# Optimization experiments

Hardware: AMD Instinct MI355X
Metric: run time of the kernel (lower is better)

## Reference

```python
import jax, jax.numpy as jnp
import numpy as np
from jax.scipy.linalg import cho_solve, solve_triangular

O = 9            # observations per timestep
L1S1, L1S2 = 3, 1
L = L1S1 + L1S2  # latent dim = 4
N, NT = 4096, 400
JITTER = 1e-6
EPS = 1e-9
LOG2PI = float(np.log(2.0 * np.pi))


def setup_inputs():
    key = jax.random.key(0)
    ks = jax.random.split(key, 9)
    return {
        "y": jax.random.normal(ks[0], (N, NT, O), jnp.float32),
        "B1_state1": 0.3 * jax.random.normal(ks[1], (L1S1, L1S1), jnp.float32),
        "B1_state2": 0.3 * jax.random.normal(ks[2], (L1S2, L1S2), jnp.float32),
        "lambda_r1_free": 0.8 + 0.1 * jax.random.normal(ks[3], (6,), jnp.float32),
        "lambda_r2_free": 0.8 + 0.1 * jax.random.normal(ks[4], (8,), jnp.float32),
        "log_q_diag": 0.1 * jax.random.normal(ks[5], (L,), jnp.float32),
        "log_r_diag": 0.1 * jax.random.normal(ks[6], (O,), jnp.float32),
        "gamma_intercept": 0.5 + 0.1 * jax.random.normal(ks[7], (1,), jnp.float32),
        "gamma_coeffs": 0.1 * jax.random.normal(ks[8], (3,), jnp.float32),
    }


def _build_matrices(B1_state1, B1_state2, l1f, l2f, log_q, log_r):
    B = (jnp.zeros((L, L), jnp.float32)
         .at[:L1S1, :L1S1].set(B1_state1)
         .at[L1S1:, L1S1:].set(B1_state2))
    Q = jnp.diag(jnp.exp(log_q))
    R = jnp.diag(jnp.exp(log_r))
    L1 = (jnp.zeros((O, L), jnp.float32)
          .at[0, 0].set(1.0).at[1, 0].set(l1f[0]).at[2, 0].set(l1f[1])
          .at[3, 1].set(1.0).at[4, 1].set(l1f[2]).at[5, 1].set(l1f[3])
          .at[6, 2].set(1.0).at[7, 2].set(l1f[4]).at[8, 2].set(l1f[5]))
    L2 = jnp.zeros((O, L), jnp.float32).at[0, L1S1].set(1.0).at[1:, L1S1].set(l2f)
    return B, Q, R, L1, L2


def _imm_kf(y, B1_state1, B1_state2, lambda_r1_free, lambda_r2_free,
            log_q_diag, log_r_diag, gamma_intercept, gamma_coeffs):
    n = y.shape[0]
    B, Q, R, L1, L2 = _build_matrices(B1_state1, B1_state2, lambda_r1_free,
                                      lambda_r2_free, log_q_diag, log_r_diag)
    eyeL = jnp.eye(L, dtype=jnp.float32)
    eyeO = jnp.eye(O, dtype=jnp.float32)

    def regime_update(y_t, eta_pred, P_pred, Lm):
        # One regime's Kalman update + Gaussian log-likelihood of the innovation.
        v = y_t - eta_pred @ Lm.T                        # [N,O]
        LP = jnp.einsum('oi,nij->noj', Lm, P_pred)       # [N,O,L]
        F = LP @ Lm.T + R + JITTER * eyeO                # [N,O,O] innovation cov
        c = jnp.linalg.cholesky(F)
        z = solve_triangular(c, v[..., None], lower=True)[..., 0]
        log_lik = (-0.5 * O * LOG2PI
                   - jnp.log(jnp.diagonal(c, axis1=-2, axis2=-1)).sum(-1)
                   - 0.5 * (z * z).sum(-1))              # [N]
        # K = P_pred L^T F^{-1}; F symmetric so K^T = F^{-1} L P_pred
        K = jnp.swapaxes(cho_solve((c, True), LP), -1, -2)   # [N,L,O]
        eta_u = eta_pred + (K @ v[..., None])[..., 0]
        A = eyeL - K @ Lm                                # Joseph form
        P_u = (A @ P_pred @ jnp.swapaxes(A, -1, -2)
               + jnp.einsum('nlo,op,nmp->nlm', K, R, K))
        return log_lik, eta_u, P_u

    def step(carry, y_t):
        prob, eta, P, ll = carry
        p11 = jax.nn.sigmoid(gamma_intercept[0] + eta[:, :L1S1] @ gamma_coeffs)
        eta_pred = eta @ B.T                             # [N,L]
        P_pred = jnp.einsum('ij,njk,lk->nil', B, P, B) + Q
        ll1, eta1, P1 = regime_update(y_t, eta_pred, P_pred, L1)
        ll2, eta2, P2 = regime_update(y_t, eta_pred, P_pred, L2)
        num1 = jnp.exp(ll1) * (prob[:, 0] * p11)                        # p21 = 0
        num2 = jnp.exp(ll2) * (prob[:, 0] * (1.0 - p11) + prob[:, 1])   # p22 = 1
        marg = num1 + num2 + EPS
        pr1, pr2 = num1 / marg, num2 / marg
        ll = ll + jnp.log(marg).sum()
        eta_t = pr1[:, None] * eta1 + pr2[:, None] * eta2
        d1 = (eta1 - eta_t)[..., None]
        d2 = (eta2 - eta_t)[..., None]
        P_t = (pr1[:, None, None] * (P1 + d1 @ jnp.swapaxes(d1, -1, -2))
               + pr2[:, None, None] * (P2 + d2 @ jnp.swapaxes(d2, -1, -2)))
        P_t = 0.5 * (P_t + jnp.swapaxes(P_t, -1, -2))
        probs_t = jnp.stack([pr1, pr2], axis=-1)
        y_pred = pr1[:, None] * (eta_t @ L1.T) + pr2[:, None] * (eta_t @ L2.T)
        return (probs_t, eta_t, P_t, ll), (probs_t, y_pred)

    prob0 = jnp.broadcast_to(jnp.array([0.99, 0.01], jnp.float32), (n, 2))
    eta0 = jnp.zeros((n, L), jnp.float32)
    P0 = jnp.broadcast_to(1000.0 * eyeL, (n, L, L))
    (_, _, _, ll), (probs, y_pred) = jax.lax.scan(
        step, (prob0, eta0, P0, jnp.asarray(0.0, jnp.float32)),
        jnp.swapaxes(y, 0, 1))
    # (neg log-likelihood, filtered_probs [N,Nt,2], predicted_y [N,Nt,O])
    return -ll, jnp.swapaxes(probs, 0, 1), jnp.swapaxes(y_pred, 0, 1)


def reference(y, B1_state1, B1_state2, lambda_r1_free, lambda_r2_free,
              log_q_diag, log_r_diag, gamma_intercept, gamma_coeffs):
    return _imm_kf(y, B1_state1, B1_state2, lambda_r1_free, lambda_r2_free,
                   log_q_diag, log_r_diag, gamma_intercept, gamma_coeffs)
```

## Files before the change

### kernel.cpp

```cpp
#include <hip/hip_runtime.h>
#include <math.h>

#define N_PART 4096
#define N_T    400
#define N_O    9
#define NJ     (N_T*N_O)
#define TT     20
#define LOG2PI_F 1.8378770664093453f

typedef float v2f __attribute__((ext_vector_type(2)));

__device__ __forceinline__ v2f v2exp(v2f x){ v2f r; r.x=__expf(x.x); r.y=__expf(x.y); return r; }
__device__ __forceinline__ v2f v2log(v2f x){ v2f r; r.x=__logf(x.x); r.y=__logf(x.y); return r; }
__device__ __forceinline__ v2f v2rcp(v2f x){ v2f r; r.x=__builtin_amdgcn_rcpf(x.x); r.y=__builtin_amdgcn_rcpf(x.y); return r; }

__global__ __launch_bounds__(256)
void transpose_kernel(const float* __restrict__ y, float* __restrict__ yt,
                      float* __restrict__ ll_ws)
{
    __shared__ float tile[64][65];
    if (blockIdx.x == 0 && blockIdx.y == 0 && threadIdx.x == 0) ll_ws[0] = 0.0f;
    const int j0 = blockIdx.x * 64;
    const int n0 = blockIdx.y * 64;
    const int c  = threadIdx.x & 63;
    const int r4 = threadIdx.x >> 6;
#pragma unroll
    for (int k = 0; k < 16; ++k) {
        const int rr = r4 + 4*k;
        const int j  = j0 + c;
        if (j < NJ) tile[rr][c] = y[(size_t)(n0 + rr) * NJ + j];
    }
    __syncthreads();
#pragma unroll
    for (int k = 0; k < 16; ++k) {
        const int rr = r4 + 4*k;
        const int j  = j0 + rr;
        if (j < NJ) yt[(size_t)j * N_PART + n0 + c] = tile[c][rr];
    }
}

#define STEP(YC, T, OWN) do {                                                     \
    const v2f xg  = gi + e0*gc0 + e1*gc1 + e2*gc2;                                \
    const v2f p11 = v2rcp(1.0f + v2exp(-xg));                                     \
    const v2f ep0 = B00*e0 + B01*e1 + B02*e2;                                     \
    const v2f ep1 = B10*e0 + B11*e1 + B12*e2;                                     \
    const v2f ep2 = B20*e0 + B21*e1 + B22*e2;                                     \
    const v2f ep3 = b2*e3;                                                        \
    const v2f C00 = B00*P00 + B01*P01 + B02*P02;                                  \
    const v2f C01 = B00*P01 + B01*P11 + B02*P12;                                  \
    const v2f C02 = B00*P02 + B01*P12 + B02*P22;                                  \
    const v2f C10 = B10*P00 + B11*P01 + B12*P02;                                  \
    const v2f C11 = B10*P01 + B11*P11 + B12*P12;                                  \
    const v2f C12 = B10*P02 + B11*P12 + B12*P22;                                  \
    const v2f C20 = B20*P00 + B21*P01 + B22*P02;                                  \
    const v2f C21 = B20*P01 + B21*P11 + B22*P12;                                  \
    const v2f C22 = B20*P02 + B21*P12 + B22*P22;                                  \
    const v2f Pp00 = C00*B00 + C01*B01 + C02*B02 + q0;                            \
    const v2f Pp01 = C00*B10 + C01*B11 + C02*B12;                                 \
    const v2f Pp02 = C00*B20 + C01*B21 + C02*B22;                                 \
    const v2f Pp11 = C10*B10 + C11*B11 + C12*B12 + q1;                            \
    const v2f Pp12 = C10*B20 + C11*B21 + C12*B22;                                 \
    const v2f Pp22 = C20*B20 + C21*B21 + C22*B22 + q2;                            \
    const v2f Pp03 = b2*(B00*P03 + B01*P13 + B02*P23);                            \
    const v2f Pp13 = b2*(B10*P03 + B11*P13 + B12*P23);                            \
    const v2f Pp23 = b2*(B20*P03 + B21*P13 + B22*P23);                            \
    const v2f Pp33 = b2*b2*P33 + q3;                                              \
    v2f v1[9];                                                                    \
    v1[0]=YC[0]-lam1[0]*ep0; v1[1]=YC[1]-lam1[1]*ep0; v1[2]=YC[2]-lam1[2]*ep0;    \
    v1[3]=YC[3]-lam1[3]*ep1; v1[4]=YC[4]-lam1[4]*ep1; v1[5]=YC[5]-lam1[5]*ep1;    \
    v1[6]=YC[6]-lam1[6]*ep2; v1[7]=YC[7]-lam1[7]*ep2; v1[8]=YC[8]-lam1[8]*ep2;    \
    v2f vRv1 = {0,0};                                                             \
    _Pragma("unroll")                                                             \
    for (int o = 0; o < 9; ++o) vRv1 += v1[o]*v1[o]*ri[o];                        \
    const v2f b0  = aA[0]*v1[0] + aA[1]*v1[1] + aA[2]*v1[2];                      \
    const v2f b1  = aA[3]*v1[3] + aA[4]*v1[4] + aA[5]*v1[5];                      \
    const v2f bb2 = aA[6]*v1[6] + aA[7]*v1[7] + aA[8]*v1[8];                      \
    const v2f A00 = 1.0f + gA0*Pp00, A01 = gA0*Pp01, A02 = gA0*Pp02;              \
    const v2f A10 = gA1*Pp01, A11 = 1.0f + gA1*Pp11, A12 = gA1*Pp12;              \
    const v2f A20 = gA2*Pp02, A21 = gA2*Pp12, A22 = 1.0f + gA2*Pp22;              \
    const v2f c00 = A11*A22 - A12*A21;                                            \
    const v2f c01 = A12*A20 - A10*A22;                                            \
    const v2f c02 = A10*A21 - A11*A20;                                            \
    const v2f det = A00*c00 + A01*c01 + A02*c02;                                  \
    const v2f idet = v2rcp(det);                                                  \
    const v2f Ai00 = c00*idet;                                                    \
    const v2f Ai01 = (A02*A21 - A01*A22)*idet;                                    \
    const v2f Ai02 = (A01*A12 - A02*A11)*idet;                                    \
    const v2f Ai10 = c01*idet;                                                    \
    const v2f Ai11 = (A00*A22 - A02*A20)*idet;                                    \
    const v2f Ai12 = (A02*A10 - A00*A12)*idet;                                    \
    const v2f Ai20 = c02*idet;                                                    \
    const v2f Ai21 = (A01*A20 - A00*A21)*idet;                                    \
    const v2f Ai22 = (A00*A11 - A01*A10)*idet;                                    \
    const v2f u0 = Ai00*b0 + Ai01*b1 + Ai02*bb2;                                  \
    const v2f u1 = Ai10*b0 + Ai11*b1 + Ai12*bb2;                                  \
    const v2f uu2= Ai20*b0 + Ai21*b1 + Ai22*bb2;                                  \
    const v2f sb0 = Pp00*b0 + Pp01*b1 + Pp02*bb2;                                 \
    const v2f sb1 = Pp01*b0 + Pp11*b1 + Pp12*bb2;                                 \
    const v2f sb2 = Pp02*b0 + Pp12*b1 + Pp22*bb2;                                 \
    const v2f qf1 = vRv1 - (u0*sb0 + u1*sb1 + uu2*sb2);                           \
    const v2f ll1 = -0.5f*(llconst + v2log(det) + qf1);                           \
    const v2f W00 = Ai00*gA0, W01 = Ai01*gA1, W02 = Ai02*gA2;                     \
    const v2f W11 = Ai11*gA1, W12 = Ai12*gA2, W22 = Ai22*gA2;                     \
    const v2f r00=Pp00, r01=Pp01, r02=Pp02;                                       \
    const v2f r10=Pp01, r11=Pp11, r12=Pp12;                                       \
    const v2f r20=Pp02, r21=Pp12, r22=Pp22;                                       \
    const v2f r30=Pp03, r31=Pp13, r32=Pp23;                                       \
    const v2f eta1_0 = ep0 + r00*u0 + r01*u1 + r02*uu2;                           \
    const v2f eta1_1 = ep1 + r10*u0 + r11*u1 + r12*uu2;                           \
    const v2f eta1_2 = ep2 + r20*u0 + r21*u1 + r22*uu2;                           \
    const v2f eta1_3 = ep3 + r30*u0 + r31*u1 + r32*uu2;                           \
    const v2f Jg00=r00*W00+r01*W01+r02*W02, Jg01=r00*W01+r01*W11+r02*W12, Jg02=r00*W02+r01*W12+r02*W22; \
    const v2f Jg10=r10*W00+r11*W01+r12*W02, Jg11=r10*W01+r11*W11+r12*W12, Jg12=r10*W02+r11*W12+r12*W22; \
    const v2f Jg20=r20*W00+r21*W01+r22*W02, Jg21=r20*W01+r21*W11+r22*W12, Jg22=r20*W02+r21*W12+r22*W22; \
    const v2f Jg30=r30*W00+r31*W01+r32*W02, Jg31=r30*W01+r31*W11+r32*W12, Jg32=r30*W02+r31*W12+r32*W22; \
    const v2f P1_00 = Pp00 - (Jg00*r00 + Jg01*r01 + Jg02*r02);                    \
    const v2f P1_01 = Pp01 - (Jg00*r10 + Jg01*r11 + Jg02*r12);                    \
    const v2f P1_02 = Pp02 - (Jg00*r20 + Jg01*r21 + Jg02*r22);                    \
    const v2f P1_03 = Pp03 - (Jg00*r30 + Jg01*r31 + Jg02*r32);                    \
    const v2f P1_11 = Pp11 - (Jg10*r10 + Jg11*r11 + Jg12*r12);                    \
    const v2f P1_12 = Pp12 - (Jg10*r20 + Jg11*r21 + Jg12*r22);                    \
    const v2f P1_13 = Pp13 - (Jg10*r30 + Jg11*r31 + Jg12*r32);                    \
    const v2f P1_22 = Pp22 - (Jg20*r20 + Jg21*r21 + Jg22*r22);                    \
    const v2f P1_23 = Pp23 - (Jg20*r30 + Jg21*r31 + Jg22*r32);                    \
    const v2f P1_33 = Pp33 - (Jg30*r30 + Jg31*r31 + Jg32*r32);                    \
    v2f vRv2 = {0,0}, bv2 = {0,0};                                                \
    _Pragma("unroll")                                                             \
    for (int o = 0; o < 9; ++o) {                                                 \
        const v2f v2o = YC[o] - lam2[o]*ep3;                                      \
        vRv2 += v2o*v2o*ri[o];                                                    \
        bv2  += cB[o]*v2o;                                                        \
    }                                                                             \
    const v2f s22 = Pp33;                                                         \
    const v2f d2  = 1.0f + s22*gB;                                                \
    const v2f id2 = v2rcp(d2);                                                    \
    const v2f qf2 = vRv2 - s22*id2*bv2*bv2;                                       \
    const v2f ll2 = -0.5f*(llconst + v2log(d2) + qf2);                            \
    const v2f kv  = bv2*id2;                                                      \
    const v2f eta2_0 = ep0 + Pp03*kv;                                             \
    const v2f eta2_1 = ep1 + Pp13*kv;                                             \
    const v2f eta2_2 = ep2 + Pp23*kv;                                             \
    const v2f eta2_3 = ep3 + Pp33*kv;                                             \
    const v2f beta = gB*id2;                                                      \
    const v2f bp0 = beta*Pp03, bp1 = beta*Pp13, bp2 = beta*Pp23, bp3 = beta*Pp33; \
    const v2f P2_00 = Pp00 - bp0*Pp03;                                            \
    const v2f P2_01 = Pp01 - bp0*Pp13;                                            \
    const v2f P2_02 = Pp02 - bp0*Pp23;                                            \
    const v2f P2_03 = Pp03 - bp0*Pp33;                                            \
    const v2f P2_11 = Pp11 - bp1*Pp13;                                            \
    const v2f P2_12 = Pp12 - bp1*Pp23;                                            \
    const v2f P2_13 = Pp13 - bp1*Pp33;                                            \
    const v2f P2_22 = Pp22 - bp2*Pp23;                                            \
    const v2f P2_23 = Pp23 - bp2*Pp33;                                            \
    const v2f P2_33 = Pp33 - bp3*Pp33;                                            \
    const v2f ex1 = v2exp(ll1), ex2 = v2exp(ll2);                                 \
    const v2f num1 = ex1 * (pr1 * p11);                                           \
    const v2f num2 = ex2 * (pr1 * (1.0f - p11) + pr2);                            \
    const v2f marg = num1 + num2 + 1e-9f;                                         \
    const v2f im   = v2rcp(marg);                                                 \
    const v2f w1   = num1 * im;                                                   \
    const v2f w2m  = num2 * im;                                                   \
    if (OWN) { llacc += v2log(marg); }                                            \
    const v2f et0 = w1*eta1_0 + w2m*eta2_0;                                       \
    const v2f et1 = w1*eta1_1 + w2m*eta2_1;                                       \
    const v2f et2 = w1*eta1_2 + w2m*eta2_2;                                       \
    const v2f et3 = w1*eta1_3 + w2m*eta2_3;                                       \
    const v2f d1_0 = eta1_0-et0, d1_1 = eta1_1-et1, d1_2 = eta1_2-et2, d1_3 = eta1_3-et3; \
    const v2f d2_0 = eta2_0-et0, d2_1 = eta2_1-et1, d2_2 = eta2_2-et2, d2_3 = eta2_3-et3; \
    const v2f wd1_0=w1*d1_0, wd1_1=w1*d1_1, wd1_2=w1*d1_2, wd1_3=w1*d1_3;         \
    const v2f wd2_0=w2m*d2_0, wd2_1=w2m*d2_1, wd2_2=w2m*d2_2, wd2_3=w2m*d2_3;     \
    P00 = w1*P1_00 + w2m*P2_00 + wd1_0*d1_0 + wd2_0*d2_0;                         \
    P01 = w1*P1_01 + w2m*P2_01 + wd1_0*d1_1 + wd2_0*d2_1;                         \
    P02 = w1*P1_02 + w2m*P2_02 + wd1_0*d1_2 + wd2_0*d2_2;                         \
    P03 = w1*P1_03 + w2m*P2_03 + wd1_0*d1_3 + wd2_0*d2_3;                         \
    P11 = w1*P1_11 + w2m*P2_11 + wd1_1*d1_1 + wd2_1*d2_1;                         \
    P12 = w1*P1_12 + w2m*P2_12 + wd1_1*d1_2 + wd2_1*d2_2;                         \
    P13 = w1*P1_13 + w2m*P2_13 + wd1_1*d1_3 + wd2_1*d2_3;                         \
    P22 = w1*P1_22 + w2m*P2_22 + wd1_2*d1_2 + wd2_2*d2_2;                         \
    P23 = w1*P1_23 + w2m*P2_23 + wd1_2*d1_3 + wd2_2*d2_3;                         \
    P33 = w1*P1_33 + w2m*P2_33 + wd1_3*d1_3 + wd2_3*d2_3;                         \
    e0 = et0; e1 = et1; e2 = et2; e3 = et3;                                       \
    pr1 = w1; pr2 = w2m;                                                          \
    if (OWN) {                                                                    \
        v2f* rp = recv + (size_t)(T)*6*2048;                                      \
        rp[0] = w1; rp[2048] = w2m; rp[2*2048] = et0;                             \
        rp[3*2048] = et1; rp[4*2048] = et2; rp[5*2048] = et3;                     \
    }                                                                             \
} while (0)

#define REFILL(BUF, TN) do {                                                      \
    const int tc = ((TN) < N_T) ? (TN) : N_T - 1;                                 \
    const v2f* src = ytv + (size_t)tc * 9 * 2048;                                 \
    _Pragma("unroll")                                                             \
    for (int o = 0; o < 9; ++o) BUF[o] = src[o * 2048];                           \
} while (0)

__global__ __launch_bounds__(64)
void imm_kf_kernel(const float* yt,
                   const float* __restrict__ B1s1,
                   const float* __restrict__ B1s2,
                   const float* __restrict__ l1f,
                   const float* __restrict__ l2f,
                   const float* __restrict__ log_q,
                   const float* __restrict__ log_r,
                   const float* __restrict__ gip,
                   const float* __restrict__ gcp,
                   float* rec,
                   float* __restrict__ ll_ws,
                   int segmented)
{
    const int s = segmented ? (blockIdx.x >> 5) : 0;
    const int g = segmented ? (blockIdx.x & 31) : blockIdx.x;
    const int n = g * 64 + threadIdx.x;

    int own_start, own_end, t0;
    if (!segmented)   { own_start = 0;             own_end = N_T;            t0 = 0; }
    else if (s == 0)  { own_start = 0;             own_end = 28;             t0 = 0; }
    else              { own_start = 28 + 12*(s-1); own_end = own_start + 12; t0 = own_start - 16; }

    float B00=B1s1[0],B01=B1s1[1],B02=B1s1[2];
    float B10=B1s1[3],B11=B1s1[4],B12=B1s1[5];
    float B20=B1s1[6],B21=B1s1[7],B22=B1s1[8];
    const float b2 = B1s2[0];

    float lam1[9], lam2[9];
    lam1[0]=1.0f; lam1[1]=l1f[0]; lam1[2]=l1f[1];
    lam1[3]=1.0f; lam1[4]=l1f[2]; lam1[5]=l1f[3];
    lam1[6]=1.0f; lam1[7]=l1f[4]; lam1[8]=l1f[5];
    lam2[0]=1.0f;
#pragma unroll
    for (int o = 1; o < 9; ++o) lam2[o] = l2f[o-1];

    float q0=expf(log_q[0]), q1=expf(log_q[1]), q2=expf(log_q[2]), q3=expf(log_q[3]);

    float ri[9], aA[9], cB[9];
    float logdetR = 0.0f;
    float gA0=0.f, gA1=0.f, gA2=0.f, gB=0.f;
#pragma unroll
    for (int o = 0; o < 9; ++o) {
        const float rr  = expf(log_r[o]);
        const float rj  = rr + 1e-6f;
        const float riv = 1.0f / rj;
        ri[o] = riv;
        logdetR += logf(rj);
        aA[o] = lam1[o] * riv;
        cB[o] = lam2[o] * riv;
        const float ga = lam1[o]*aA[o];
        if (o < 3) gA0 += ga; else if (o < 6) gA1 += ga; else gA2 += ga;
        gB += lam2[o]*cB[o];
    }
    const float gi  = gip[0];
    const float gc0 = gcp[0], gc1 = gcp[1], gc2 = gcp[2];
    const float llconst = 9.0f * LOG2PI_F + logdetR;

    v2f P00={1000.f,1000.f}, P01={0,0}, P02={0,0}, P03={0,0};
    v2f P11={1000.f,1000.f}, P12={0,0}, P13={0,0};
    v2f P22={1000.f,1000.f}, P23={0,0};
    v2f P33={1000.f,1000.f};
    v2f e0={0,0}, e1={0,0}, e2={0,0}, e3={0,0};
    v2f pr1={0.99f,0.99f}, pr2={0.01f,0.01f};
    v2f llacc={0,0};

    const v2f* ytv  = (const v2f*)yt + n;
    v2f*       recv = (v2f*)rec + n;

    v2f ya[9], yb[9];
    REFILL(ya, t0); REFILL(yb, t0 + 1);

    for (int t = t0; t < own_start; t += 2) {
        STEP(ya, t, 0);       REFILL(ya, t + 2);
        STEP(yb, t + 1, 0);   REFILL(yb, t + 3);
    }
    for (int t = own_start; t < own_end; t += 2) {
        STEP(ya, t, 1);       REFILL(ya, t + 2);
        STEP(yb, t + 1, 1);   REFILL(yb, t + 3);
    }

    float lls = llacc.x + llacc.y;
#pragma unroll
    for (int off = 32; off > 0; off >>= 1)
        lls += __shfl_down(lls, off, 64);
    if (threadIdx.x == 0) atomicAdd(ll_ws, lls);
}

__global__ __launch_bounds__(256)
void expand_kernel(const float* __restrict__ l1f, const float* __restrict__ l2f,
                   const float* __restrict__ rec,
                   float* __restrict__ ypred, float* __restrict__ probs,
                   const float* __restrict__ ll_ws, float* __restrict__ out0)
{
    __shared__ float tile[TT*6][66];
    __shared__ float slam[18];
    const int tid = threadIdx.x;
    const int l   = tid & 63, rq = tid >> 6;
    const int p0  = blockIdx.x * 64;
    const int t0  = blockIdx.y * TT;

    if (blockIdx.x == 0 && blockIdx.y == 0 && tid == 0) out0[0] = -ll_ws[0];

    if (tid < 18) {
        float v;
        if (tid < 9) v = (tid % 3 == 0) ? 1.0f : l1f[tid - 1 - tid/3];
        else         v = (tid == 9)     ? 1.0f : l2f[tid - 10];
        slam[tid] = v;
    }

    const float* rbase = rec + (size_t)(t0 * 6) * N_PART + p0 + l;
#pragma unroll
    for (int m = 0; m < (TT*6)/4; ++m) {
        tile[rq + 4*m][l] = rbase[(size_t)(rq + 4*m) * N_PART];
    }
    __syncthreads();

#pragma unroll
    for (int k = 0; k < TT/4; ++k) {
        float* r0 = &tile[(rq + 4*k)*6][0] + l;
        const float w1=r0[0], w2=r0[66], ee0=r0[2*66], ee1=r0[3*66], ee2=r0[4*66], ee3=r0[5*66];
        r0[2*66]=w1*ee0; r0[3*66]=w1*ee1; r0[4*66]=w1*ee2; r0[5*66]=w2*ee3;
    }
    __syncthreads();

    float* yout = ypred + (size_t)p0 * (N_T*N_O) + (size_t)t0 * N_O;
#pragma unroll 2
    for (int k = 0; k < (64*TT*9)/256; ++k) {
        const int f  = k*256 + tid;
        const int p  = f / (TT*9);
        const int j  = f - p*(TT*9);
        const int t_ = j / 9;
        const int o  = j - t_*9;
        const float v = slam[o]*tile[t_*6 + 2 + o/3][p] + slam[9+o]*tile[t_*6 + 5][p];
        yout[(size_t)p * (N_T*N_O) + j] = v;
    }

    float* pout = probs + (size_t)p0 * (N_T*2) + (size_t)t0 * 2;
#pragma unroll 2
    for (int k = 0; k < (64*TT*2)/256; ++k) {
        const int f = k*256 + tid;
        const int p = f / (TT*2);
        const int j = f - p*(TT*2);
        pout[(size_t)p * (N_T*2) + j] = tile[(j>>1)*6 + (j&1)][p];
    }
}

extern "C" void kernel_launch(void* const* d_in, const int* in_sizes, int n_in,
                              void* d_out, int out_size, void* d_ws, size_t ws_size,
                              hipStream_t stream)
{
    const float* y    = (const float*)d_in[0];
    const float* B1s1 = (const float*)d_in[1];
    const float* B1s2 = (const float*)d_in[2];
    const float* l1f  = (const float*)d_in[3];
    const float* l2f  = (const float*)d_in[4];
    const float* lq   = (const float*)d_in[5];
    const float* lr   = (const float*)d_in[6];
    const float* gi   = (const float*)d_in[7];
    const float* gc   = (const float*)d_in[8];

    float* out   = (float*)d_out;
    float* probs = out + 1;
    float* ypred = out + 1 + (size_t)N_PART * N_T * 2;
    float* ws    = (float*)d_ws;
    float* yt    = ws + 16;

    const size_t ytfl   = (size_t)NJ * N_PART;
    const size_t recfl  = (size_t)N_T * 6 * N_PART;
    const size_t need_sep = (16 + ytfl + recfl) * sizeof(float);

    transpose_kernel<<<dim3((NJ + 63)/64, N_PART/64), 256, 0, stream>>>(y, yt, ws);

    if (ws_size >= need_sep) {
        float* rec = yt + ytfl;
        imm_kf_kernel<<<1024, 64, 0, stream>>>(yt, B1s1, B1s2, l1f, l2f,
                                               lq, lr, gi, gc, rec, ws, 1);
        expand_kernel<<<dim3(N_PART/64, N_T/TT), 256, 0, stream>>>(
            l1f, l2f, rec, ypred, probs, ws, out);
    } else {
        float* rec = yt;
        imm_kf_kernel<<<32, 64, 0, stream>>>(yt, B1s1, B1s2, l1f, l2f,
                                             lq, lr, gi, gc, rec, ws, 0);
        expand_kernel<<<dim3(N_PART/64, N_T/TT), 256, 0, stream>>>(
            l1f, l2f, rec, ypred, probs, ws, out);
    }
}
```

Baseline: 206.5 us.

## Fuse output expansion into filter kernel via shared-memory chunk buffer

Removes the separate expand kernel and the global rec intermediate. Each filter block now stages its per-timestep weights and means in shared memory and writes ypred and probs directly in chunks of 12 steps. The final log-likelihood is published by the last finishing block, tracked with an atomic counter. This saves a launch and a round trip of the intermediate through global memory. In exchange, the 64-thread filter blocks take on the strided output stores and extra barriers, and a non-transposed fallback path that reads y directly is added.

```diff
diff --git a/kernel.cpp b/kernel.cpp
--- a/kernel.cpp
+++ b/kernel.cpp
@@ -5,7 +5,6 @@
 #define N_T    400
 #define N_O    9
 #define NJ     (N_T*N_O)
-#define TT     20
 #define LOG2PI_F 1.8378770664093453f
 
 typedef float v2f __attribute__((ext_vector_type(2)));
@@ -19,7 +18,7 @@
                       float* __restrict__ ll_ws)
 {
     __shared__ float tile[64][65];
-    if (blockIdx.x == 0 && blockIdx.y == 0 && threadIdx.x == 0) ll_ws[0] = 0.0f;
+    if (blockIdx.x == 0 && blockIdx.y == 0 && threadIdx.x == 0) { ll_ws[0] = 0.0f; ll_ws[1] = 0.0f; }
     const int j0 = blockIdx.x * 64;
     const int n0 = blockIdx.y * 64;
     const int c  = threadIdx.x & 63;
@@ -37,6 +36,47 @@
         const int j  = j0 + rr;
         if (j < NJ) yt[(size_t)j * N_PART + n0 + c] = tile[c][rr];
     }
+}
+
+template<int LEN>
+__device__ __forceinline__ void flush_chunk(float (*lbuf)[130], const float* slam,
+                                            float* __restrict__ ypred,
+                                            float* __restrict__ probs,
+                                            int p0, int c0, int lane)
+{
+    __syncthreads();
+#pragma unroll 4
+    for (int k = 0; k < LEN*2; ++k) {
+        const int i  = k*64 + lane;
+        const int t_ = i >> 7;
+        const int c  = i & 127;
+        const float w1 = lbuf[t_*6+0][c], w2 = lbuf[t_*6+1][c];
+        lbuf[t_*6+2][c] *= w1;
+        lbuf[t_*6+3][c] *= w1;
+        lbuf[t_*6+4][c] *= w1;
+        lbuf[t_*6+5][c] *= w2;
+    }
+    __syncthreads();
+    float* yb_ = ypred + (size_t)p0 * (N_T*N_O) + (size_t)c0 * N_O;
+#pragma unroll 4
+    for (int k = 0; k < LEN*18; ++k) {
+        const int i  = k*64 + lane;
+        const int p  = i / (LEN*9);
+        const int j  = i - p*(LEN*9);
+        const int t_ = j / 9;
+        const int o  = j - 9*t_;
+        const float v = slam[o]*lbuf[t_*6 + 2 + o/3][p] + slam[9+o]*lbuf[t_*6 + 5][p];
+        yb_[(size_t)p * (N_T*N_O) + j] = v;
+    }
+    float* pb_ = probs + (size_t)p0 * (N_T*2) + (size_t)c0 * 2;
+#pragma unroll 4
+    for (int k = 0; k < LEN*4; ++k) {
+        const int i = k*64 + lane;
+        const int p = i / (LEN*2);
+        const int j = i - p*(LEN*2);
+        pb_[(size_t)p * (N_T*2) + j] = lbuf[(j>>1)*6 + (j&1)][p];
+    }
+    __syncthreads();
 }
 
 #define STEP(YC, T, OWN) do {                                                     \
@@ -182,19 +222,28 @@
     e0 = et0; e1 = et1; e2 = et2; e3 = et3;                                       \
     pr1 = w1; pr2 = w2m;                                                          \
     if (OWN) {                                                                    \
-        v2f* rp = recv + (size_t)(T)*6*2048;                                      \
-        rp[0] = w1; rp[2048] = w2m; rp[2*2048] = et0;                             \
-        rp[3*2048] = et1; rp[4*2048] = et2; rp[5*2048] = et3;                     \
+        float* lp = &lbuf[(T)*6][0] + 2*lane;                                     \
+        *(v2f*)&lp[0]     = w1;  *(v2f*)&lp[130]   = w2m;                         \
+        *(v2f*)&lp[2*130] = et0; *(v2f*)&lp[3*130] = et1;                         \
+        *(v2f*)&lp[4*130] = et2; *(v2f*)&lp[5*130] = et3;                         \
     }                                                                             \
 } while (0)
 
 #define REFILL(BUF, TN) do {                                                      \
     const int tc = ((TN) < N_T) ? (TN) : N_T - 1;                                 \
-    const v2f* src = ytv + (size_t)tc * 9 * 2048;                                 \
-    _Pragma("unroll")                                                             \
-    for (int o = 0; o < 9; ++o) BUF[o] = src[o * 2048];                           \
+    if (TRANS) {                                                                  \
+        const v2f* src = ytv + (size_t)tc * 9 * 2048;                             \
+        _Pragma("unroll")                                                         \
+        for (int o = 0; o < 9; ++o) BUF[o] = src[o * 2048];                       \
+    } else {                                                                      \
+        _Pragma("unroll")                                                         \
+        for (int o = 0; o < 9; ++o) {                                             \
+            BUF[o].x = yA[(size_t)tc*9 + o]; BUF[o].y = yB[(size_t)tc*9 + o];     \
+        }                                                                         \
+    }                                                                             \
 } while (0)
 
+template<bool TRANS>
 __global__ __launch_bounds__(64)
 void imm_kf_kernel(const float* yt,
                    const float* __restrict__ B1s1,
@@ -205,18 +254,30 @@
                    const float* __restrict__ log_r,
                    const float* __restrict__ gip,
                    const float* __restrict__ gcp,
-                   float* rec,
-                   float* __restrict__ ll_ws,
-                   int segmented)
+                   float* __restrict__ ypred,
+                   float* __restrict__ probs,
+                   float* ll_ws,
+                   float* __restrict__ out0)
 {
-    const int s = segmented ? (blockIdx.x >> 5) : 0;
-    const int g = segmented ? (blockIdx.x & 31) : blockIdx.x;
-    const int n = g * 64 + threadIdx.x;
+    __shared__ float lbuf[12*6][130];
+    __shared__ float slam[18];
+
+    const int lane = threadIdx.x;
+    const int s = blockIdx.x >> 5;
+    const int g = blockIdx.x & 31;
+    const int n = g * 64 + lane;
+    const int p0 = g * 128;
+
+    if (lane < 18) {
+        float v;
+        if (lane < 9) v = (lane % 3 == 0) ? 1.0f : l1f[lane - 1 - lane/3];
+        else          v = (lane == 9)     ? 1.0f : l2f[lane - 10];
+        slam[lane] = v;
+    }
 
     int own_start, own_end, t0;
-    if (!segmented)   { own_start = 0;             own_end = N_T;            t0 = 0; }
-    else if (s == 0)  { own_start = 0;             own_end = 28;             t0 = 0; }
-    else              { own_start = 28 + 12*(s-1); own_end = own_start + 12; t0 = own_start - 16; }
+    if (s == 0) { own_start = 0;             own_end = 28;             t0 = 0; }
+    else        { own_start = 28 + 12*(s-1); own_end = own_start + 12; t0 = own_start - 16; }
 
     float B00=B1s1[0],B01=B1s1[1],B02=B1s1[2];
     float B10=B1s1[3],B11=B1s1[4],B12=B1s1[5];
@@ -261,84 +322,39 @@
     v2f pr1={0.99f,0.99f}, pr2={0.01f,0.01f};
     v2f llacc={0,0};
 
-    const v2f* ytv  = (const v2f*)yt + n;
-    v2f*       recv = (v2f*)rec + n;
+    const v2f*  ytv = (const v2f*)yt + n;
+    const float* yA = yt + (size_t)(2*n) * NJ;
+    const float* yB = yA + NJ;
 
     v2f ya[9], yb[9];
     REFILL(ya, t0); REFILL(yb, t0 + 1);
 
     for (int t = t0; t < own_start; t += 2) {
-        STEP(ya, t, 0);       REFILL(ya, t + 2);
-        STEP(yb, t + 1, 0);   REFILL(yb, t + 3);
-    }
-    for (int t = own_start; t < own_end; t += 2) {
-        STEP(ya, t, 1);       REFILL(ya, t + 2);
-        STEP(yb, t + 1, 1);   REFILL(yb, t + 3);
+        STEP(ya, 0, 0);       REFILL(ya, t + 2);
+        STEP(yb, 0, 0);       REFILL(yb, t + 3);
+    }
+    for (int c0 = own_start; c0 < own_end; c0 += 12) {
+        const int ce = (c0 + 12 < own_end) ? c0 + 12 : own_end;
+        for (int t = c0; t < ce; t += 2) {
+            STEP(ya, t - c0, 1);       REFILL(ya, t + 2);
+            STEP(yb, t - c0 + 1, 1);   REFILL(yb, t + 3);
+        }
+        if (ce - c0 == 12) flush_chunk<12>(lbuf, slam, ypred, probs, p0, c0, lane);
+        else               flush_chunk<4> (lbuf, slam, ypred, probs, p0, c0, lane);
     }
 
     float lls = llacc.x + llacc.y;
 #pragma unroll
     for (int off = 32; off > 0; off >>= 1)
         lls += __shfl_down(lls, off, 64);
-    if (threadIdx.x == 0) atomicAdd(ll_ws, lls);
-}
-
-__global__ __launch_bounds__(256)
-void expand_kernel(const float* __restrict__ l1f, const float* __restrict__ l2f,
-                   const float* __restrict__ rec,
-                   float* __restrict__ ypred, float* __restrict__ probs,
-                   const float* __restrict__ ll_ws, float* __restrict__ out0)
-{
-    __shared__ float tile[TT*6][66];
-    __shared__ float slam[18];
-    const int tid = threadIdx.x;
-    const int l   = tid & 63, rq = tid >> 6;
-    const int p0  = blockIdx.x * 64;
-    const int t0  = blockIdx.y * TT;
-
-    if (blockIdx.x == 0 && blockIdx.y == 0 && tid == 0) out0[0] = -ll_ws[0];
-
-    if (tid < 18) {
-        float v;
-        if (tid < 9) v = (tid % 3 == 0) ? 1.0f : l1f[tid - 1 - tid/3];
-        else         v = (tid == 9)     ? 1.0f : l2f[tid - 10];
-        slam[tid] = v;
-    }
-
-    const float* rbase = rec + (size_t)(t0 * 6) * N_PART + p0 + l;
-#pragma unroll
-    for (int m = 0; m < (TT*6)/4; ++m) {
-        tile[rq + 4*m][l] = rbase[(size_t)(rq + 4*m) * N_PART];
-    }
-    __syncthreads();
-
-#pragma unroll
-    for (int k = 0; k < TT/4; ++k) {
-        float* r0 = &tile[(rq + 4*k)*6][0] + l;
-        const float w1=r0[0], w2=r0[66], ee0=r0[2*66], ee1=r0[3*66], ee2=r0[4*66], ee3=r0[5*66];
-        r0[2*66]=w1*ee0; r0[3*66]=w1*ee1; r0[4*66]=w1*ee2; r0[5*66]=w2*ee3;
-    }
-    __syncthreads();
-
-    float* yout = ypred + (size_t)p0 * (N_T*N_O) + (size_t)t0 * N_O;
-#pragma unroll 2
-    for (int k = 0; k < (64*TT*9)/256; ++k) {
-        const int f  = k*256 + tid;
-        const int p  = f / (TT*9);
-        const int j  = f - p*(TT*9);
-        const int t_ = j / 9;
-        const int o  = j - t_*9;
-        const float v = slam[o]*tile[t_*6 + 2 + o/3][p] + slam[9+o]*tile[t_*6 + 5][p];
-        yout[(size_t)p * (N_T*N_O) + j] = v;
-    }
-
-    float* pout = probs + (size_t)p0 * (N_T*2) + (size_t)t0 * 2;
-#pragma unroll 2
-    for (int k = 0; k < (64*TT*2)/256; ++k) {
-        const int f = k*256 + tid;
-        const int p = f / (TT*2);
-        const int j = f - p*(TT*2);
-        pout[(size_t)p * (N_T*2) + j] = tile[(j>>1)*6 + (j&1)][p];
+    if (lane == 0) {
+        atomicAdd(ll_ws, lls);
+        __threadfence();
+        unsigned prev = atomicAdd((unsigned*)(ll_ws + 1), 1u);
+        if (prev == gridDim.x - 1) {
+            __threadfence();
+            out0[0] = -ll_ws[0];
+        }
     }
 }
 
@@ -362,23 +378,18 @@
     float* ws    = (float*)d_ws;
     float* yt    = ws + 16;
 
-    const size_t ytfl   = (size_t)NJ * N_PART;
-    const size_t recfl  = (size_t)N_T * 6 * N_PART;
-    const size_t need_sep = (16 + ytfl + recfl) * sizeof(float);
-
-    transpose_kernel<<<dim3((NJ + 63)/64, N_PART/64), 256, 0, stream>>>(y, yt, ws);
-
-    if (ws_size >= need_sep) {
-        float* rec = yt + ytfl;
-        imm_kf_kernel<<<1024, 64, 0, stream>>>(yt, B1s1, B1s2, l1f, l2f,
-                                               lq, lr, gi, gc, rec, ws, 1);
-        expand_kernel<<<dim3(N_PART/64, N_T/TT), 256, 0, stream>>>(
-            l1f, l2f, rec, ypred, probs, ws, out);
+    const size_t ytfl = (size_t)NJ * N_PART;
+    const size_t need = (16 + ytfl) * sizeof(float);
+
+    if (ws_size >= need) {
+        transpose_kernel<<<dim3((NJ + 63)/64, N_PART/64), 256, 0, stream>>>(y, yt, ws);
+        imm_kf_kernel<true><<<1024, 64, 0, stream>>>(yt, B1s1, B1s2, l1f, l2f,
+                                                     lq, lr, gi, gc,
+                                                     ypred, probs, ws, out);
     } else {
-        float* rec = yt;
-        imm_kf_kernel<<<32, 64, 0, stream>>>(yt, B1s1, B1s2, l1f, l2f,
-                                             lq, lr, gi, gc, rec, ws, 0);
-        expand_kernel<<<dim3(N_PART/64, N_T/TT), 256, 0, stream>>>(
-            l1f, l2f, rec, ypred, probs, ws, out);
+        hipMemsetAsync(ws, 0, 2*sizeof(float), stream);
+        imm_kf_kernel<false><<<1024, 64, 0, stream>>>(y, B1s1, B1s2, l1f, l2f,
+                                                      lq, lr, gi, gc,
+                                                      ypred, probs, ws, out);
     }
 }
```

Result: slower. 236.5 us (+14.5%).
